# Kernel optimization log

Measured on AMD Instinct MI355X. Metric: run time of the kernel, lower is better.

## Reference

```python
import jax, jax.numpy as jnp
import numpy as np

B, N, C = 8, 1024, 768
DIM_HEAD = 32
NUM_HEADS = C // DIM_HEAD  # 24


def setup_inputs() -> dict:
    key = jax.random.key(0)
    ks = jax.random.split(key, 6)
    s = 0.02
    return {
        "x": jax.random.normal(ks[0], (B, N, C), dtype=jnp.float32),
        "shared_rel_pos": jax.random.normal(ks[1], (NUM_HEADS, N, N), dtype=jnp.float32),
        "Wqkv": jax.random.normal(ks[2], (3 * C, C), dtype=jnp.float32) * s,
        "bqkv": jax.random.normal(ks[3], (3 * C,), dtype=jnp.float32) * s,
        "Wproj": jax.random.normal(ks[4], (C, C), dtype=jnp.float32) * s,
        "bproj": jax.random.normal(ks[5], (C,), dtype=jnp.float32) * s,
    }


def reference(x, shared_rel_pos, Wqkv, bqkv, Wproj, bproj):
    b, n, c = x.shape
    h, dh = NUM_HEADS, DIM_HEAD
    scale = dh ** -0.5
    # qkv projection: [B,N,3C] -> view as [B,N,H,3*dh] (head_first layout)
    qkv = (jnp.einsum('bnc,oc->bno', x, Wqkv) + bqkv).reshape(b, n, h, 3 * dh)
    qkv = jnp.transpose(qkv, (0, 2, 1, 3))          # [B,H,N,3*dh]
    q, k, v = jnp.split(qkv, 3, axis=-1)            # each [B,H,N,dh]
    attn = jnp.einsum('bhqd,bhkd->bhqk', q * scale, k)  # [B,H,N,N]
    attn = attn + shared_rel_pos[None]              # broadcast bias [H,N,N]
    attn = jax.nn.softmax(attn, axis=-1)
    out = jnp.einsum('bhqk,bhkd->bhqd', attn, v)    # [B,H,N,dh]
    out = jnp.transpose(out, (0, 2, 1, 3)).reshape(b, n, h * dh)
    return jnp.einsum('bnc,oc->bno', out, Wproj) + bproj
```

## Files before the change

kernel.cpp:

```cpp
#include <hip/hip_runtime.h>

typedef __bf16 bf16_t;
typedef __bf16 bf16x8 __attribute__((ext_vector_type(8)));
typedef __bf16 bf16x4 __attribute__((ext_vector_type(4)));
typedef float f32x4 __attribute__((ext_vector_type(4)));

#define MFMA16(a, b, c) __builtin_amdgcn_mfma_f32_16x16x32_bf16(a, b, c, 0, 0, 0)

#if __has_builtin(__builtin_amdgcn_exp2f)
#define EXP2(x) __builtin_amdgcn_exp2f(x)
#else
#define EXP2(x) exp2f(x)
#endif

__device__ __forceinline__ void g2l16(const void* g, void* l) {
  __builtin_amdgcn_global_load_lds(
      (__attribute__((address_space(1))) void*)g,
      (__attribute__((address_space(3))) void*)l, 16, 0, 0);
}

__global__ void cvt_f32_bf16(const float* __restrict__ in, bf16_t* __restrict__ out, int n4) {
  int i = blockIdx.x * blockDim.x + threadIdx.x;
  if (i >= n4) return;
  const float4 v = ((const float4*)in)[i];
  bf16x4 o;
  o[0] = (bf16_t)v.x; o[1] = (bf16_t)v.y; o[2] = (bf16_t)v.z; o[3] = (bf16_t)v.w;
  ((bf16x4*)out)[i] = o;
}

__global__ void permute_rel(const float* __restrict__ rel, bf16_t* __restrict__ relp) {
  __shared__ float row[1024];
  const size_t base = (size_t)blockIdx.x * 1024;
  const int t = threadIdx.x;
  *(float4*)(row + t * 4) = *(const float4*)(rel + base + t * 4);
  __syncthreads();
  const float LOG2E = 1.44269504f;
  const int o0 = t * 4;
  bf16x4 v;
#pragma unroll
  for (int j = 0; j < 4; ++j) {
    const int o = o0 + j;
    const int kb = o >> 7, rem = o & 127;
    const int lr = rem >> 3, jt = rem & 7;
    v[j] = (bf16_t)(row[kb * 128 + jt * 16 + lr] * LOG2E);
  }
  *(bf16x4*)(relp + base + o0) = v;
}

__global__ void transpose_v(const bf16_t* __restrict__ Vb, bf16_t* __restrict__ Vtb) {
  __shared__ bf16_t T[64][40];
  const int bh = blockIdx.y, s0 = blockIdx.x * 64;
  const int r = threadIdx.x >> 2, c8 = (threadIdx.x & 3) * 8;
  const bf16x8 v = *(const bf16x8*)(Vb + ((size_t)bh * 1024 + s0 + r) * 32 + c8);
#pragma unroll
  for (int j = 0; j < 8; ++j) T[r][c8 + j] = v[j];
  __syncthreads();
  const int d = threadIdx.x >> 3, q8 = (threadIdx.x & 7) * 8;
  bf16x8 o;
#pragma unroll
  for (int j = 0; j < 8; ++j) o[j] = T[q8 + j][d];
  *(bf16x8*)(Vtb + ((size_t)bh * 32 + d) * 1024 + s0 + q8) = o;
}

template <int MODE>
__global__ __launch_bounds__(256, 2) void gemm_bt(
    const bf16_t* __restrict__ A, const bf16_t* __restrict__ Bw,
    const float* __restrict__ bias, float* __restrict__ Cout,
    bf16_t* __restrict__ Qb, bf16_t* __restrict__ Kb, bf16_t* __restrict__ Vb,
    int M, int N, int K) {
  __shared__ bf16_t As[128 * 32];
  __shared__ bf16_t Bs[128 * 32];
  const int tid = threadIdx.x;
  const int wave = tid >> 6, lane = tid & 63, quad = lane >> 4, lr = lane & 15;
  const int bm = blockIdx.x * 128, bn = blockIdx.y * 128;
  const int wm = (wave >> 1) * 64, wn = (wave & 1) * 64;

  f32x4 acc[4][4] = {};

  const bf16_t* Ag;
  size_t strideA64;
  if (MODE == 0) {
    Ag = A + (size_t)(bm + (tid >> 2)) * K + (tid & 3) * 8;
    strideA64 = (size_t)64 * K;
  } else {
    const int rr = bm + (tid >> 2);
    const int bidx = rr >> 10, seq = rr & 1023;
    Ag = A + ((size_t)bidx * 24 * 1024 + seq) * 32 + (tid & 3) * 8;
    strideA64 = (size_t)64 * 32;
  }
  const bf16_t* Bg = Bw + (size_t)(bn + (tid >> 2)) * K + (tid & 3) * 8;
  bf16_t* As0 = As + tid * 8;
  bf16_t* Bs0 = Bs + tid * 8;
  const size_t strideB64 = (size_t)64 * K;

  for (int k0 = 0; k0 < K; k0 += 32) {
    const size_t aoff = (MODE == 0) ? (size_t)k0 : (size_t)(k0 >> 5) * 32768;
    __syncthreads();
    g2l16(Ag + aoff, As0);
    g2l16(Ag + strideA64 + aoff, As0 + 2048);
    g2l16(Bg + k0, Bs0);
    g2l16(Bg + strideB64 + k0, Bs0 + 2048);
    __syncthreads();
    bf16x8 af[4], bfr[4];
#pragma unroll
    for (int i = 0; i < 4; ++i)
      af[i] = *(const bf16x8*)(As + (wm + i * 16 + lr) * 32 + quad * 8);
#pragma unroll
    for (int j = 0; j < 4; ++j)
      bfr[j] = *(const bf16x8*)(Bs + (wn + j * 16 + lr) * 32 + quad * 8);
#pragma unroll
    for (int i = 0; i < 4; ++i)
#pragma unroll
      for (int j = 0; j < 4; ++j)
        acc[i][j] = MFMA16(af[i], bfr[j], acc[i][j]);
  }

#pragma unroll
  for (int i = 0; i < 4; ++i) {
    const int row = bm + wm + i * 16 + quad * 4;
#pragma unroll
    for (int j = 0; j < 4; ++j) {
      const int col = bn + wn + j * 16 + lr;
      const float bb = bias[col];
#pragma unroll
      for (int r = 0; r < 4; ++r) {
        const float v = acc[i][j][r] + bb;
        const int rr = row + r;
        if (MODE == 1) {
          Cout[(size_t)rr * N + col] = v;
        } else {
          const int b = rr >> 10, seq = rr & 1023;
          const int head = col / 96, w = col % 96;
          const int bh = b * 24 + head;
          if (w < 32) {
            Qb[((size_t)bh * 1024 + seq) * 32 + w] = (bf16_t)(v * 0.17677669529663687f);
          } else if (w < 64) {
            Kb[((size_t)bh * 1024 + seq) * 32 + (w - 32)] = (bf16_t)v;
          } else {
            Vb[((size_t)bh * 1024 + seq) * 32 + (w - 64)] = (bf16_t)v;
          }
        }
      }
    }
  }
}

__global__ __launch_bounds__(256, 4) void attn_flash(
    const bf16_t* __restrict__ Qb, const bf16_t* __restrict__ Kb,
    const bf16_t* __restrict__ Vtb, const bf16_t* __restrict__ relp,
    bf16_t* __restrict__ Ob) {
  __shared__ bf16_t Ks[2][128 * 32];
  __shared__ bf16_t Vs[2][32 * 128];
  __shared__ bf16_t Ps[4][16 * 132];

  const int tid = threadIdx.x;
  const int wave = tid >> 6, lane = tid & 63, quad = lane >> 4, lr = lane & 15;

  const int flat = blockIdx.x;
  const int xcd = flat & 7, slot = flat >> 3;
  const int pair = xcd + 8 * (slot >> 4);
  const int qi = slot & 15;
  const int b = pair / 24, h = pair % 24;
  const int bh = b * 24 + h;
  const int q0 = qi * 64 + wave * 16;
  const float LOG2E = 1.44269504f;

  const bf16x8 qf = *(const bf16x8*)(Qb + ((size_t)bh * 1024 + q0 + lr) * 32 + quad * 8);

  bf16x8 onesf;
#pragma unroll
  for (int i = 0; i < 8; ++i) onesf[i] = (bf16_t)1.0f;

  f32x4 o_acc[2] = {};
  f32x4 l_acc = {};

  const bf16_t* relg = relp + ((size_t)h * 1024 + q0 + quad * 4) * 1024 + lr * 8;
  const bf16_t* Kg = Kb + (size_t)bh * 1024 * 32;
  const bf16_t* Vg = Vtb + (size_t)bh * 32 * 1024;
  bf16_t* Pw = &Ps[wave][0];

  auto stageKV = [&](int kt, int sel) {
#pragma unroll
    for (int p = 0; p < 2; ++p) {
      const int cid = p * 256 + tid;
      const int krow = cid >> 2, kc = cid & 3;
      const int ks_ = (krow >> 1) & 3;
      g2l16(Kg + ((size_t)(kt + krow) * 32 + ((kc ^ ks_) * 8)), &Ks[sel][cid * 8]);
      const int vd = cid >> 4, vc = cid & 15;
      g2l16(Vg + ((size_t)vd * 1024 + kt + ((vc ^ (vd & 7)) * 8)), &Vs[sel][cid * 8]);
    }
  };

  auto body = [&](int kt, int sel) {
    bf16x8 bw[4];
    const bf16_t* rb = relg + kt;
#pragma unroll
    for (int r = 0; r < 4; ++r) bw[r] = *(const bf16x8*)(rb + (size_t)r * 1024);

    f32x4 s[8];
    const f32x4 zz = {0.f, 0.f, 0.f, 0.f};
    const int kcs = quad ^ ((lr >> 1) & 3);
#pragma unroll
    for (int jt = 0; jt < 8; ++jt) {
      const int row = jt * 16 + lr;
      const bf16x8 kf = *(const bf16x8*)&Ks[sel][row * 32 + kcs * 8];
      s[jt] = MFMA16(qf, kf, zz);
    }
#pragma unroll
    for (int jt = 0; jt < 8; ++jt)
#pragma unroll
      for (int r = 0; r < 4; ++r)
        s[jt][r] = EXP2(fmaf(s[jt][r], LOG2E, (float)bw[r][jt]));

#pragma unroll
    for (int jt = 0; jt < 8; ++jt)
#pragma unroll
      for (int r = 0; r < 4; ++r)
        Pw[(quad * 4 + r) * 132 + jt * 16 + lr] = (bf16_t)s[jt][r];

#pragma unroll
    for (int ks = 0; ks < 4; ++ks) {
      const bf16x8 pf = *(const bf16x8*)(Pw + lr * 132 + ks * 32 + quad * 8);
      l_acc = MFMA16(pf, onesf, l_acc);
#pragma unroll
      for (int nt = 0; nt < 2; ++nt) {
        const int d = nt * 16 + lr;
        const int vc = (ks * 4 + quad) ^ (d & 7);
        const bf16x8 vf = *(const bf16x8*)&Vs[sel][d * 128 + vc * 8];
        o_acc[nt] = MFMA16(pf, vf, o_acc[nt]);
      }
    }
  };

  stageKV(0, 0);
  __syncthreads();
  for (int t = 0; t < 8; ++t) {
    const int sel = t & 1;
    if (t < 7) stageKV((t + 1) * 128, sel ^ 1);
    body(t * 128, sel);
    __syncthreads();
  }

  float inv_l[4];
#pragma unroll
  for (int r = 0; r < 4; ++r) inv_l[r] = 1.0f / l_acc[r];
#pragma unroll
  for (int nt = 0; nt < 2; ++nt)
#pragma unroll
    for (int r = 0; r < 4; ++r) {
      const int seq = q0 + quad * 4 + r;
      Ob[((size_t)bh * 1024 + seq) * 32 + nt * 16 + lr] = (bf16_t)(o_acc[nt][r] * inv_l[r]);
    }
}

extern "C" void kernel_launch(void* const* d_in, const int* in_sizes, int n_in,
                              void* d_out, int out_size, void* d_ws, size_t ws_size,
                              hipStream_t stream) {
  const float* x = (const float*)d_in[0];
  const float* rel = (const float*)d_in[1];
  const float* Wqkv = (const float*)d_in[2];
  const float* bqkv = (const float*)d_in[3];
  const float* Wproj = (const float*)d_in[4];
  const float* bproj = (const float*)d_in[5];
  float* out = (float*)d_out;

  char* ws = (char*)d_ws;
  bf16_t* xb = (bf16_t*)ws;     ws += (size_t)8192 * 768 * 2;
  bf16_t* wqkvb = (bf16_t*)ws;  ws += (size_t)2304 * 768 * 2;
  bf16_t* wprojb = (bf16_t*)ws; ws += (size_t)768 * 768 * 2;
  bf16_t* Qb = (bf16_t*)ws;     ws += (size_t)192 * 1024 * 32 * 2;
  bf16_t* Kb = (bf16_t*)ws;     ws += (size_t)192 * 1024 * 32 * 2;
  bf16_t* Vb = (bf16_t*)ws;     ws += (size_t)192 * 1024 * 32 * 2;
  bf16_t* Vtb = (bf16_t*)ws;    ws += (size_t)192 * 1024 * 32 * 2;
  bf16_t* relp = (bf16_t*)ws;   ws += (size_t)24 * 1024 * 1024 * 2;
  bf16_t* Ob = xb;

  cvt_f32_bf16<<<(8192 * 768 / 4 + 255) / 256, 256, 0, stream>>>(x, xb, 8192 * 768 / 4);
  cvt_f32_bf16<<<(2304 * 768 / 4 + 255) / 256, 256, 0, stream>>>(Wqkv, wqkvb, 2304 * 768 / 4);
  cvt_f32_bf16<<<(768 * 768 / 4 + 255) / 256, 256, 0, stream>>>(Wproj, wprojb, 768 * 768 / 4);
  permute_rel<<<dim3(24 * 1024), 256, 0, stream>>>(rel, relp);

  gemm_bt<0><<<dim3(64, 18), 256, 0, stream>>>(xb, wqkvb, bqkv, nullptr,
                                               Qb, Kb, Vb, 8192, 2304, 768);
  transpose_v<<<dim3(16, 192), 256, 0, stream>>>(Vb, Vtb);
  attn_flash<<<dim3(3072), 256, 0, stream>>>(Qb, Kb, Vtb, relp, Ob);
  gemm_bt<1><<<dim3(64, 6), 256, 0, stream>>>(Ob, wprojb, bproj, out,
                                              nullptr, nullptr, nullptr, 8192, 768, 768);
}
```

Before: 369.1 us.

## Pre-permute bias into per-lane MFMA fragment layout and transpose score tile

The relative-position bias is now re-laid out in 16-query tiles so each lane of a wave reads its bias fragment as contiguous 16-byte vectors. Previously each lane gathered four strided rows. The QK^T MFMA operands are swapped so scores come out transposed, which lets P be written to LDS as packed 4-element vectors instead of scalar stores. The P row pitch changes to 136 to match. The aim is cheaper bias loads and fewer LDS store instructions in the attention inner loop, at the cost of a more complex permute kernel and a tight coupling of the two layouts.

```diff
diff --git a/kernel.cpp b/kernel.cpp
--- a/kernel.cpp
+++ b/kernel.cpp
@@ -29,22 +29,37 @@
 }
 
 __global__ void permute_rel(const float* __restrict__ rel, bf16_t* __restrict__ relp) {
-  __shared__ float row[1024];
-  const size_t base = (size_t)blockIdx.x * 1024;
+  __shared__ bf16_t Tl[16][1032];
+  const int blk = blockIdx.x;
+  const int h = blk >> 6, qt = blk & 63;
   const int t = threadIdx.x;
-  *(float4*)(row + t * 4) = *(const float4*)(rel + base + t * 4);
+  const float LOG2E = 1.44269504f;
+  const float* src = rel + ((size_t)h * 1024 + qt * 16) * 1024;
+#pragma unroll
+  for (int it = 0; it < 16; ++it) {
+    const int fid = it * 256 + t;
+    const int row = fid >> 8, c4 = (fid & 255) * 4;
+    const float4 v = *(const float4*)(src + (size_t)row * 1024 + c4);
+    bf16x4 o;
+    o[0] = (bf16_t)(v.x * LOG2E); o[1] = (bf16_t)(v.y * LOG2E);
+    o[2] = (bf16_t)(v.z * LOG2E); o[3] = (bf16_t)(v.w * LOG2E);
+    *(bf16x4*)&Tl[row][c4] = o;
+  }
   __syncthreads();
-  const float LOG2E = 1.44269504f;
-  const int o0 = t * 4;
-  bf16x4 v;
-#pragma unroll
-  for (int j = 0; j < 4; ++j) {
-    const int o = o0 + j;
-    const int kb = o >> 7, rem = o & 127;
-    const int lr = rem >> 3, jt = rem & 7;
-    v[j] = (bf16_t)(row[kb * 128 + jt * 16 + lr] * LOG2E);
-  }
-  *(bf16x4*)(relp + base + o0) = v;
+  bf16_t* dst = relp + (size_t)blk * 16384;
+#pragma unroll
+  for (int s = 0; s < 8; ++s) {
+    const int c = s * 256 + t;
+    const int kb = c >> 8, i = (c >> 6) & 3, lane = c & 63;
+    const int lr = lane & 15, quad = lane >> 4;
+    bf16x8 o;
+#pragma unroll
+    for (int j = 0; j < 8; ++j) {
+      const int k = kb * 128 + (2 * i + (j >> 2)) * 16 + quad * 4 + (j & 3);
+      o[j] = Tl[lr][k];
+    }
+    *(bf16x8*)(dst + (size_t)c * 8) = o;
+  }
 }
 
 __global__ void transpose_v(const bf16_t* __restrict__ Vb, bf16_t* __restrict__ Vtb) {
@@ -151,7 +166,7 @@
     bf16_t* __restrict__ Ob) {
   __shared__ bf16_t Ks[2][128 * 32];
   __shared__ bf16_t Vs[2][32 * 128];
-  __shared__ bf16_t Ps[4][16 * 132];
+  __shared__ bf16_t Ps[4][16 * 136];
 
   const int tid = threadIdx.x;
   const int wave = tid >> 6, lane = tid & 63, quad = lane >> 4, lr = lane & 15;
@@ -174,7 +189,7 @@
   f32x4 o_acc[2] = {};
   f32x4 l_acc = {};
 
-  const bf16_t* relg = relp + ((size_t)h * 1024 + q0 + quad * 4) * 1024 + lr * 8;
+  const bf16_t* relg = relp + (size_t)(h * 64 + qi * 4 + wave) * 16384 + lane * 8;
   const bf16_t* Kg = Kb + (size_t)bh * 1024 * 32;
   const bf16_t* Vg = Vtb + (size_t)bh * 32 * 1024;
   bf16_t* Pw = &Ps[wave][0];
@@ -192,35 +207,37 @@
   };
 
   auto body = [&](int kt, int sel) {
-    bf16x8 bw[4];
-    const bf16_t* rb = relg + kt;
-#pragma unroll
-    for (int r = 0; r < 4; ++r) bw[r] = *(const bf16x8*)(rb + (size_t)r * 1024);
+    bf16x8 bb[4];
+    const bf16_t* rb = relg + (size_t)(kt >> 7) * 2048;
+#pragma unroll
+    for (int i = 0; i < 4; ++i) bb[i] = *(const bf16x8*)(rb + i * 512);
 
     f32x4 s[8];
     const f32x4 zz = {0.f, 0.f, 0.f, 0.f};
     const int kcs = quad ^ ((lr >> 1) & 3);
 #pragma unroll
     for (int jt = 0; jt < 8; ++jt) {
-      const int row = jt * 16 + lr;
-      const bf16x8 kf = *(const bf16x8*)&Ks[sel][row * 32 + kcs * 8];
-      s[jt] = MFMA16(qf, kf, zz);
+      const bf16x8 kf = *(const bf16x8*)&Ks[sel][(jt * 16 + lr) * 32 + kcs * 8];
+      s[jt] = MFMA16(kf, qf, zz);
     }
 #pragma unroll
     for (int jt = 0; jt < 8; ++jt)
 #pragma unroll
       for (int r = 0; r < 4; ++r)
-        s[jt][r] = EXP2(fmaf(s[jt][r], LOG2E, (float)bw[r][jt]));
-
-#pragma unroll
-    for (int jt = 0; jt < 8; ++jt)
-#pragma unroll
-      for (int r = 0; r < 4; ++r)
-        Pw[(quad * 4 + r) * 132 + jt * 16 + lr] = (bf16_t)s[jt][r];
-
+        s[jt][r] = EXP2(fmaf(s[jt][r], LOG2E, (float)bb[jt >> 1][(jt & 1) * 4 + r]));
+
+#pragma unroll
+    for (int jt = 0; jt < 8; ++jt) {
+      bf16x4 p4;
+      p4[0] = (bf16_t)s[jt][0]; p4[1] = (bf16_t)s[jt][1];
+      p4[2] = (bf16_t)s[jt][2]; p4[3] = (bf16_t)s[jt][3];
+      *(bf16x4*)&Pw[lr * 136 + jt * 16 + quad * 4] = p4;
+    }
+
+    const bf16_t* Vbase = Vg + kt;
 #pragma unroll
     for (int ks = 0; ks < 4; ++ks) {
-      const bf16x8 pf = *(const bf16x8*)(Pw + lr * 132 + ks * 32 + quad * 8);
+      const bf16x8 pf = *(const bf16x8*)&Pw[lr * 136 + ks * 32 + quad * 8];
       l_acc = MFMA16(pf, onesf, l_acc);
 #pragma unroll
       for (int nt = 0; nt < 2; ++nt) {
@@ -278,7 +295,7 @@
   cvt_f32_bf16<<<(8192 * 768 / 4 + 255) / 256, 256, 0, stream>>>(x, xb, 8192 * 768 / 4);
   cvt_f32_bf16<<<(2304 * 768 / 4 + 255) / 256, 256, 0, stream>>>(Wqkv, wqkvb, 2304 * 768 / 4);
   cvt_f32_bf16<<<(768 * 768 / 4 + 255) / 256, 256, 0, stream>>>(Wproj, wprojb, 768 * 768 / 4);
-  permute_rel<<<dim3(24 * 1024), 256, 0, stream>>>(rel, relp);
+  permute_rel<<<dim3(24 * 64), 256, 0, stream>>>(rel, relp);
 
   gemm_bt<0><<<dim3(64, 18), 256, 0, stream>>>(xb, wqkvb, bqkv, nullptr,
                                                Qb, Kb, Vb, 8192, 2304, 768);
```

Result: faster. 355.1 us (-3.8%).
